# Performance work log

Hardware: AMD Instinct MI355X
Metric: run time of the kernel (lower is better)

Reference implementation:

```python
import jax, jax.numpy as jnp
import numpy as np

DIM = 256
EXP = 4
EPS_DYT = 1e-5
EPS_ATTN = 1e-5
TEMP = 10000.0


def _linear(x, w, b):
    # torch nn.Linear: y = x @ W^T + b, W is [out, in]
    return jnp.einsum('...i,oi->...o', x, w) + b


def _dwconv3x3(x_nhwc, w, b):
    # depthwise 3x3, padding=1; w: [C,1,3,3]
    xc = x_nhwc.transpose(0, 3, 1, 2)
    y = jax.lax.conv_general_dilated(
        xc, w, window_strides=(1, 1), padding='SAME',
        feature_group_count=w.shape[0],
        dimension_numbers=('NCHW', 'OIHW', 'NCHW'))
    return y.transpose(0, 2, 3, 1) + b


def _dyt(x, gamma, beta):
    mu = x.mean(axis=-1, keepdims=True)
    sd = x.std(axis=-1, keepdims=True, ddof=1) + EPS_DYT  # torch std is unbiased
    return jnp.tanh(gamma * (x - mu) / sd + beta)


def _mona(x, w, b):
    # SE-style: global avg pool -> fc -> sigmoid -> channel gate
    s = jax.nn.sigmoid(_linear(x.mean(axis=(1, 2)), w, b))  # [B,C]
    return x * s[:, None, None, :]


def _pos_emb(H, W, C):
    dq = C // 4
    omega = 1.0 / (TEMP ** (jnp.arange(dq, dtype=jnp.float32) / dq))
    xo = jnp.arange(W, dtype=jnp.float32)[:, None] * omega  # [W,dq]
    yo = jnp.arange(H, dtype=jnp.float32)[:, None] * omega  # [H,dq]
    xe = jnp.concatenate([jnp.sin(xo), jnp.cos(xo)], axis=-1)  # [W,2dq]
    ye = jnp.concatenate([jnp.sin(yo), jnp.cos(yo)], axis=-1)  # [H,2dq]
    pos = jnp.concatenate([
        jnp.broadcast_to(xe[None, :, :], (H, W, 2 * dq)),
        jnp.broadcast_to(ye[:, None, :], (H, W, 2 * dq))], axis=-1)  # [H,W,C]
    return pos


def setup_inputs() -> dict:
    key = jax.random.key(0)
    ks = jax.random.split(key, 16)
    d = DIM
    dh = d * EXP
    w = lambda k, shape: jax.random.normal(k, shape, dtype=jnp.float32) * 0.02
    return {
        'x': jax.random.normal(ks[0], (8, d // 4, 64, 64), dtype=jnp.float32),
        'in_proj_w': w(ks[1], (d, d // 4)),
        'wq_w': w(ks[2], (d, d)), 'wq_b': jnp.zeros((d,), jnp.float32),
        'wk_w': w(ks[3], (d, d)), 'wk_b': jnp.zeros((d,), jnp.float32),
        'wv_w': w(ks[4], (d, d)), 'wv_b': jnp.zeros((d,), jnp.float32),
        'wo_w': w(ks[5], (d, d)), 'wo_b': jnp.zeros((d,), jnp.float32),
        'psi_w': w(ks[6], (d, 1, 3, 3)), 'psi_b': jnp.zeros((d,), jnp.float32),
        'dyt_g': jnp.ones((d,), jnp.float32), 'dyt_b': jnp.zeros((d,), jnp.float32),
        'm1_w': w(ks[7], (d, d)), 'm1_b': jnp.zeros((d,), jnp.float32),
        'm2_w': w(ks[8], (d, d)), 'm2_b': jnp.zeros((d,), jnp.float32),
        'we_w': w(ks[9], (dh, d)), 'we_b': jnp.zeros((dh,), jnp.float32),
        'dw_w': w(ks[10], (dh, 1, 3, 3)), 'dw_b': jnp.zeros((dh,), jnp.float32),
        'wp_w': w(ks[11], (d, dh)), 'wp_b': jnp.zeros((d,), jnp.float32),
        'out_proj_w': w(ks[12], (d // 4, d)),
    }


def _sapa(x, wq_w, wq_b, wk_w, wk_b, wv_w, wv_b, wo_w, wo_b, psi_w, psi_b):
    B, H, W, C = x.shape
    N = H * W
    pos = _pos_emb(H, W, C).reshape(N, C)
    psi = jax.nn.sigmoid(_dwconv3x3(x, psi_w, psi_b)).reshape(B, N, C)
    xf = x.reshape(B, N, C)
    Q = psi * (_linear(xf, wq_w, wq_b) + pos)
    K = psi * (_linear(xf, wk_w, wk_b) + pos)
    V = _linear(xf, wv_w, wv_b)
    phi_Q = jnp.square(jax.nn.relu(Q))
    phi_K = jnp.square(jax.nn.relu(K))
    # attn / (phiQ @ sum_n phiK + eps) @ V  ==  (phiQ @ (phiK^T V)) / (phiQ @ ksum + eps)
    kv = jnp.einsum('bnc,bnd->bcd', phi_K, V)           # [B,C,C]
    num = jnp.einsum('bnc,bcd->bnd', phi_Q, kv)         # [B,N,C]
    den = jnp.einsum('bnc,bc->bn', phi_Q, phi_K.sum(axis=1))[..., None] + EPS_ATTN
    out = _linear(num / den, wo_w, wo_b)
    return out.reshape(B, H, W, C)


def _edffn(x, we_w, we_b, dw_w, dw_b, wp_w, wp_b):
    h = _linear(x, we_w, we_b)                 # [B,H,W,4C]
    h = jax.nn.gelu(_dwconv3x3(h, dw_w, dw_b))
    return x + _linear(h, wp_w, wp_b)


def reference(x, in_proj_w, wq_w, wq_b, wk_w, wk_b, wv_w, wv_b, wo_w, wo_b,
              psi_w, psi_b, dyt_g, dyt_b, m1_w, m1_b, m2_w, m2_b,
              we_w, we_b, dw_w, dw_b, wp_w, wp_b, out_proj_w):
    # in_proj: 1x1 conv (no bias; eval-BN is identity) + SiLU -> NHWC
    h = jax.nn.silu(jnp.einsum('bchw,oc->bhwo', x, in_proj_w))
    a = _sapa(h, wq_w, wq_b, wk_w, wk_b, wv_w, wv_b, wo_w, wo_b, psi_w, psi_b)
    U1 = _mona(_dyt(h + a, dyt_g, dyt_b), m1_w, m1_b)
    U2 = U1 + _edffn(U1, we_w, we_b, dw_w, dw_b, wp_w, wp_b)
    Y = _mona(_dyt(U2, dyt_g, dyt_b), m2_w, m2_b)
    return jax.nn.silu(jnp.einsum('bhwc,oc->bohw', Y, out_proj_w))
```

## Files before the change

kernel.cpp:

```cpp
#include <hip/hip_runtime.h>
#include <hip/hip_bf16.h>
#include <cmath>

using bf16 = __hip_bfloat16;
using bf16x8 = __attribute__((ext_vector_type(8))) short;
using bf16x4 = __attribute__((ext_vector_type(4))) short;
using f32x4v = __attribute__((ext_vector_type(4))) float;

static constexpr int BB  = 8;
static constexpr int HW  = 64;
static constexpr int NN  = HW * HW;
static constexpr int CC  = 256;
static constexpr int CIN = 64;
static constexpr int DH  = 1024;
static constexpr int MM  = BB * NN;

__device__ __forceinline__ bf16 f2b(float v) { return __float2bfloat16(v); }
__device__ __forceinline__ float b2f(bf16 v) { return __bfloat162float(v); }
__device__ __forceinline__ float tf(float v) { return v; }
__device__ __forceinline__ float tf(bf16 v)  { return b2f(v); }
__device__ __forceinline__ float frcp(float x) { return __builtin_amdgcn_rcpf(x); }
__device__ __forceinline__ float sigmf(float x) { return frcp(1.f + __expf(-x)); }
__device__ __forceinline__ float siluf(float x) { return x * sigmf(x); }
__device__ __forceinline__ float geluf(float x) {
  float z = x * fmaf(x * x, 0.07135481627f, 1.5957691216f);
  return x * sigmf(z);
}
__device__ __forceinline__ float tanhfast(float x) {
  return 1.f - 2.f * frcp(1.f + __expf(2.f * x));
}

__device__ __forceinline__ void stage16(const bf16* g, bf16* l) {
  __builtin_amdgcn_global_load_lds(
      (const __attribute__((address_space(1))) void*)g,
      (__attribute__((address_space(3))) void*)l, 16, 0, 0);
}

__global__ __launch_bounds__(256) void pos_kern(float* __restrict__ pos) {
  int n = blockIdx.x, o = threadIdx.x;
  int yy = n >> 6, xx = n & 63;
  int i = o & 63, q = o >> 6;
  float omega = __expf((float)i * -0.14391156831212787f);
  float coord = (q < 2) ? (float)xx : (float)yy;
  float ang = coord * omega;
  pos[(size_t)n * CC + o] = (q & 1) ? __cosf(ang) : __sinf(ang);
}

__global__ __launch_bounds__(256) void cvt_weights(
    const float* __restrict__ wq, const float* __restrict__ wk,
    const float* __restrict__ wv, const float* __restrict__ wo,
    const float* __restrict__ we, const float* __restrict__ wp,
    const float* __restrict__ qb, const float* __restrict__ kb,
    const float* __restrict__ vb,
    bf16* __restrict__ wqkvb, bf16* __restrict__ wob,
    bf16* __restrict__ web, bf16* __restrict__ wpb,
    float* __restrict__ bqkv, float* __restrict__ ksum) {
  int i = blockIdx.x * 256 + threadIdx.x;
  switch (blockIdx.y) {
    case 0: if (i < 65536) wqkvb[i] = f2b(wq[i]);
            if (i < 2048) ksum[i] = 0.f;
            break;
    case 1: if (i < 65536) wqkvb[65536 + i] = f2b(wk[i]);
            if (i < 768) bqkv[i] = (i < 256) ? qb[i] : (i < 512) ? kb[i - 256] : vb[i - 512];
            break;
    case 2: if (i < 65536) wqkvb[131072 + i] = f2b(wv[i]); break;
    case 3: if (i < 65536) wob[i] = f2b(wo[i]); break;
    case 4: web[i] = f2b(we[i]); break;
    case 5: wpb[i] = f2b(wp[i]); break;
  }
}

__global__ __launch_bounds__(256) void inproj_tile(const float* __restrict__ X,
                                                   const float* __restrict__ W,
                                                   float* __restrict__ H,
                                                   bf16* __restrict__ Hb) {
  __shared__ float Xs[16][68];
  __shared__ float Ws[16][68];
  int m0 = blockIdx.x * 64, o0 = blockIdx.y * 64, b = blockIdx.z;
  int tid = threadIdx.x, tx = tid & 15, ty = tid >> 4;
  float acc[4][4] = {};
  for (int k0 = 0; k0 < CIN; k0 += 16) {
    {
      int mm = tid & 63, kk0 = tid >> 6;
#pragma unroll
      for (int i = 0; i < 4; ++i) {
        int kk = kk0 * 4 + i;
        Xs[kk][mm] = X[((size_t)(b * CIN + k0 + kk)) * NN + m0 + mm];
      }
    }
    {
      int kk = tid & 15, oo0 = tid >> 4;
#pragma unroll
      for (int i = 0; i < 4; ++i) {
        int oo = oo0 + i * 16;
        Ws[kk][oo] = W[(size_t)(o0 + oo) * CIN + k0 + kk];
      }
    }
    __syncthreads();
#pragma unroll
    for (int kk = 0; kk < 16; ++kk) {
      float xv[4], wv[4];
#pragma unroll
      for (int a = 0; a < 4; ++a) xv[a] = Xs[kk][ty * 4 + a];
#pragma unroll
      for (int c = 0; c < 4; ++c) wv[c] = Ws[kk][tx * 4 + c];
#pragma unroll
      for (int a = 0; a < 4; ++a)
#pragma unroll
        for (int c = 0; c < 4; ++c) acc[a][c] += xv[a] * wv[c];
    }
    __syncthreads();
  }
#pragma unroll
  for (int a = 0; a < 4; ++a) {
    int m = m0 + ty * 4 + a;
#pragma unroll
    for (int c = 0; c < 4; ++c) {
      int o = o0 + tx * 4 + c;
      float v = siluf(acc[a][c]);
      size_t idx = ((size_t)b * NN + m) * CC + o;
      H[idx] = v;
      Hb[idx] = f2b(v);
    }
  }
}

__global__ __launch_bounds__(256) void outproj_tile(const float* __restrict__ T2,
                                                    const float* __restrict__ gate,
                                                    const float* __restrict__ W,
                                                    float* __restrict__ Y) {
  __shared__ float Xs[16][68];
  __shared__ float Ws[16][68];
  int n0 = blockIdx.x * 64, b = blockIdx.z;
  size_t mbase = (size_t)b * NN;
  const float* gb = gate + b * CC;
  int tid = threadIdx.x, tx = tid & 15, ty = tid >> 4;
  float acc[4][4] = {};
  for (int k0 = 0; k0 < CC; k0 += 16) {
    int kk = tid & 15, rr0 = tid >> 4;
    float gk = gb[k0 + kk];
#pragma unroll
    for (int i = 0; i < 4; ++i) {
      int rr = rr0 + i * 16;
      Xs[kk][rr] = T2[(mbase + n0 + rr) * CC + k0 + kk] * gk;
      Ws[kk][rr] = (rr < CIN) ? W[(size_t)rr * CC + k0 + kk] : 0.f;
    }
    __syncthreads();
#pragma unroll
    for (int kk2 = 0; kk2 < 16; ++kk2) {
      float xv[4], wv[4];
#pragma unroll
      for (int a = 0; a < 4; ++a) xv[a] = Xs[kk2][ty * 4 + a];
#pragma unroll
      for (int c = 0; c < 4; ++c) wv[c] = Ws[kk2][tx * 4 + c];
#pragma unroll
      for (int a = 0; a < 4; ++a)
#pragma unroll
        for (int c = 0; c < 4; ++c) acc[a][c] += xv[a] * wv[c];
    }
    __syncthreads();
  }
#pragma unroll
  for (int a = 0; a < 4; ++a) {
    int n = n0 + ty * 4 + a;
#pragma unroll
    for (int c = 0; c < 4; ++c) {
      int o = tx * 4 + c;
      if (o < CIN)
        Y[(size_t)(b * CIN + o) * NN + n] = siluf(acc[a][c]);
    }
  }
}

enum { EPI_PLAIN = 0, EPI_BIAS = 1, EPI_NUM = 3, EPI_RESID = 4, EPI_ADD1 = 5 };

__device__ __forceinline__ void storeO(float* p, float v) { *p = v; }
__device__ __forceinline__ void storeO(bf16* p, float v) { *p = f2b(v); }

template <int EPI, bool WPB, bool KVS, bool XSWZ, typename YT, typename A2T>
__global__ __launch_bounds__(256) void gemm_bf16(const bf16* __restrict__ X,
                                                 const bf16* __restrict__ W,
                                                 const float* __restrict__ bias,
                                                 YT* __restrict__ Y, int Kd, int Od,
                                                 const float* __restrict__ aux1,
                                                 const A2T* __restrict__ aux2) {
  __shared__ __align__(16) bf16 As[128 * 32];
  __shared__ __align__(16) bf16 Bs[128 * 32];
  int m0, o0;
  if (XSWZ) {
    int gy = gridDim.y;
    int nwg = gridDim.x * gy;
    int lin = blockIdx.y * gridDim.x + blockIdx.x;
    int q = nwg >> 3;
    int lin2 = (lin & 7) * q + (lin >> 3);
    m0 = (lin2 / gy) * 128;
    o0 = (lin2 % gy) * 128;
  } else {
    m0 = blockIdx.x * 128;
    o0 = blockIdx.y * 128;
  }
  int kbeg = 0, kend = Kd;
  if (KVS) {
    int b = blockIdx.z >> 4, ks = blockIdx.z & 15;
    size_t off = (size_t)b * CC * Kd;
    X += off; W += off;
    Y += (size_t)blockIdx.z * CC * CC;
    kbeg = ks * (Kd / 16); kend = kbeg + Kd / 16;
  }
  const bf16* Wp = WPB ? (W + (size_t)(m0 >> 12) * Kd * Od) : W;
  int t = threadIdx.x;
  int l = t & 63, w = t >> 6;
  int wm = (w >> 1) * 64, wn = (w & 1) * 64;
  int lr = l & 15, lq = l >> 4;
  int srow = t >> 2, skc = (t & 3) * 8;
  f32x4v acc[4][4] = {};
  for (int k0 = kbeg; k0 < kend; k0 += 32) {
    stage16(X + (size_t)(m0 + srow) * Kd + k0 + skc, As + t * 8);
    stage16(X + (size_t)(m0 + 64 + srow) * Kd + k0 + skc, As + 2048 + t * 8);
    stage16(Wp + (size_t)(o0 + srow) * Kd + k0 + skc, Bs + t * 8);
    stage16(Wp + (size_t)(o0 + 64 + srow) * Kd + k0 + skc, Bs + 2048 + t * 8);
    __syncthreads();
    bf16x8 af[4], bfr[4];
#pragma unroll
    for (int mt = 0; mt < 4; ++mt)
      af[mt] = *(const bf16x8*)(As + (wm + mt * 16 + lr) * 32 + lq * 8);
#pragma unroll
    for (int nt = 0; nt < 4; ++nt)
      bfr[nt] = *(const bf16x8*)(Bs + (wn + nt * 16 + lr) * 32 + lq * 8);
#pragma unroll
    for (int mt = 0; mt < 4; ++mt)
#pragma unroll
      for (int nt = 0; nt < 4; ++nt)
        acc[mt][nt] = __builtin_amdgcn_mfma_f32_16x16x32_bf16(af[mt], bfr[nt], acc[mt][nt], 0, 0, 0);
    __syncthreads();
  }
#pragma unroll
  for (int nt = 0; nt < 4; ++nt) {
    int o = o0 + wn + nt * 16 + lr;
    float bv = (EPI == EPI_PLAIN || EPI == EPI_NUM) ? 0.f : bias[o];
#pragma unroll
    for (int mt = 0; mt < 4; ++mt) {
      int mb = m0 + wm + mt * 16 + lq * 4;
#pragma unroll
      for (int r = 0; r < 4; ++r) {
        int m = mb + r;
        float v = acc[mt][nt][r] + bv;
        if constexpr (EPI == EPI_PLAIN || EPI == EPI_BIAS) {
          storeO(Y + (size_t)m * Od + o, v);
        } else if constexpr (EPI == EPI_NUM) {
          storeO(Y + (size_t)m * Od + o, v * aux1[m]);
        } else if constexpr (EPI == EPI_ADD1) {
          storeO(Y + (size_t)m * Od + o, v + tf(aux2[(size_t)m * Od + o]));
        } else {
          int gb = m >> 12;
          float u1 = tf(aux2[(size_t)m * Od + o]) * aux1[gb * CC + o];
          storeO(Y + (size_t)m * Od + o, v + 2.f * u1);
        }
      }
    }
  }
}

__global__ __launch_bounds__(256) void qkmath_kern(const bf16* __restrict__ QKV,
                                                   const float* __restrict__ pose,
                                                   const bf16* __restrict__ psi,
                                                   bf16* __restrict__ PQ,
                                                   bf16* __restrict__ KT,
                                                   bf16* __restrict__ VTo,
                                                   float* __restrict__ ksum) {
  __shared__ bf16 Ts[64][258];
  int sec = blockIdx.y;
  int m0 = blockIdx.x * 64;
  int b = m0 >> 12, n0 = m0 & (NN - 1);
  int t = threadIdx.x;
  int cg = (t & 31) * 8;
  int rg = t >> 5;
  if (sec == 0) {
#pragma unroll
    for (int p = 0; p < 8; ++p) {
      int r = p * 8 + rg;
      size_t m = (size_t)m0 + r;
      int n = (int)(m & (NN - 1));
      union { bf16x8 v; bf16 e[8]; } qv, pv, ov;
      qv.v = *(const bf16x8*)(QKV + m * 768 + cg);
      pv.v = *(const bf16x8*)(psi + m * CC + cg);
      const float* pr = pose + (size_t)n * CC + cg;
      f32x4v p0 = *(const f32x4v*)pr;
      f32x4v p1 = *(const f32x4v*)(pr + 4);
#pragma unroll
      for (int j = 0; j < 8; ++j) {
        float pj = (j < 4) ? p0[j] : p1[j - 4];
        float v = (b2f(qv.e[j]) + pj) * b2f(pv.e[j]);
        v = fmaxf(v, 0.f);
        ov.e[j] = f2b(v * v);
      }
      *(bf16x8*)(PQ + m * CC + cg) = ov.v;
    }
    return;
  }
  const bool KM = (sec == 1);
#pragma unroll
  for (int p = 0; p < 8; ++p) {
    int r = p * 8 + rg;
    size_t m = (size_t)m0 + r;
    union { bf16x8 v; bf16 e[8]; } qv, ov;
    qv.v = *(const bf16x8*)(QKV + m * 768 + sec * 256 + cg);
    if (KM) {
      int n = (int)(m & (NN - 1));
      union { bf16x8 v; bf16 e[8]; } pv;
      pv.v = *(const bf16x8*)(psi + m * CC + cg);
      const float* pr = pose + (size_t)n * CC + cg;
      f32x4v p0 = *(const f32x4v*)pr;
      f32x4v p1 = *(const f32x4v*)(pr + 4);
#pragma unroll
      for (int j = 0; j < 8; ++j) {
        float pj = (j < 4) ? p0[j] : p1[j - 4];
        float v = (b2f(qv.e[j]) + pj) * b2f(pv.e[j]);
        v = fmaxf(v, 0.f);
        ov.e[j] = f2b(v * v);
      }
    } else {
      ov.v = qv.v;
    }
    *(bf16x8*)(&Ts[r][cg]) = ov.v;
  }
  __syncthreads();
  int wv = t >> 6, lane = t & 63;
  bf16* base = KM ? KT : VTo;
  int nloc = (lane & 7) * 8;
  int gsub = lane >> 3;
#pragma unroll
  for (int k = 0; k < 8; ++k) {
    int c = wv * 64 + k * 8 + gsub;
    union { bf16x8 v; bf16 e[8]; } pk;
#pragma unroll
    for (int i = 0; i < 8; ++i) pk.e[i] = Ts[nloc + i][c];
    *(bf16x8*)(base + ((size_t)(b * CC + c)) * NN + n0 + nloc) = pk.v;
    if (KM) {
      float s = 0.f;
#pragma unroll
      for (int i = 0; i < 8; ++i) s += b2f(pk.e[i]);
      s += __shfl_xor(s, 1);
      s += __shfl_xor(s, 2);
      s += __shfl_xor(s, 4);
      if ((lane & 7) == 0) atomicAdd(&ksum[b * CC + c], s);
    }
  }
}

__global__ __launch_bounds__(256) void kvred_kern(const float* __restrict__ part,
                                                  bf16* __restrict__ kvTb) {
  int d = blockIdx.x, b = blockIdx.y, c = threadIdx.x;
  float s = 0.f;
#pragma unroll
  for (int ks = 0; ks < 16; ++ks)
    s += part[((size_t)(b * 16 + ks) * CC + d) * CC + c];
  kvTb[((size_t)b * CC + d) * CC + c] = f2b(s);
}

__global__ __launch_bounds__(256) void den_kern(const bf16* __restrict__ PQ,
                                                const float* __restrict__ ksum,
                                                float* __restrict__ rden) {
  int b = blockIdx.y;
  int n = blockIdx.x * 4 + (threadIdx.x >> 6);
  int lane = threadIdx.x & 63;
  size_t m = (size_t)b * NN + n;
  union { bf16x4 v; bf16 e[4]; } u;
  u.v = *(const bf16x4*)(PQ + m * CC + lane * 4);
  const float* ks = ksum + b * CC + lane * 4;
  float s = 0.f;
#pragma unroll
  for (int j = 0; j < 4; ++j) s += b2f(u.e[j]) * ks[j];
#pragma unroll
  for (int off = 32; off >= 1; off >>= 1) s += __shfl_down(s, off);
  if (lane == 0) rden[m] = 1.f / (s + 1e-5f);
}

template <bool RESID>
__global__ __launch_bounds__(256) void dyt_kern(const float* __restrict__ X,
                                                const float* __restrict__ R,
                                                const float* __restrict__ g,
                                                const float* __restrict__ bt,
                                                float* __restrict__ T,
                                                float* __restrict__ poolq) {
  int wv = threadIdx.x >> 6;
  int m = blockIdx.x * 4 + wv;
  int lane = threadIdx.x & 63;
  size_t base = (size_t)m * CC + lane * 4;
  f32x4v x = *(const f32x4v*)(X + base);
  if constexpr (RESID) {
    f32x4v r = *(const f32x4v*)(R + base);
#pragma unroll
    for (int j = 0; j < 4; ++j) x[j] += r[j];
  }
  float s = (x[0] + x[1]) + (x[2] + x[3]);
  float q = fmaf(x[0], x[0], fmaf(x[1], x[1], fmaf(x[2], x[2], x[3] * x[3])));
#pragma unroll
  for (int off = 32; off >= 1; off >>= 1) {
    s += __shfl_xor(s, off);
    q += __shfl_xor(q, off);
  }
  float mu = s * (1.f / 256.f);
  float var = (q - 256.f * mu * mu) * (1.f / 255.f);
  float sd = sqrtf(fmaxf(var, 0.f)) + 1e-5f;
  float rs = frcp(sd);
  f32x4v gv = *(const f32x4v*)(g + lane * 4);
  f32x4v bv = *(const f32x4v*)(bt + lane * 4);
  f32x4v o;
#pragma unroll
  for (int j = 0; j < 4; ++j)
    o[j] = tanhfast(fmaf(gv[j] * (x[j] - mu), rs, bv[j]));
  *(f32x4v*)(T + base) = o;
  __shared__ float ps[4][260];
#pragma unroll
  for (int j = 0; j < 4; ++j) ps[wv][lane * 4 + j] = o[j];
  __syncthreads();
  if (wv == 0) {
    f32x4v pv;
#pragma unroll
    for (int j = 0; j < 4; ++j) {
      int c = lane * 4 + j;
      pv[j] = (ps[0][c] + ps[1][c]) + (ps[2][c] + ps[3][c]);
    }
    *(f32x4v*)(poolq + (size_t)blockIdx.x * 256 + lane * 4) = pv;
  }
}

__global__ __launch_bounds__(256) void poolred_kern(const float* __restrict__ poolq,
                                                    float* __restrict__ pool16) {
  int s = blockIdx.x, b = blockIdx.y, c = threadIdx.x;
  float acc = 0.f;
#pragma unroll 8
  for (int k = 0; k < 64; ++k)
    acc += poolq[((size_t)(b * 1024 + s * 64 + k)) * 256 + c];
  pool16[(size_t)(b * 16 + s) * 256 + c] = acc;
}

__global__ __launch_bounds__(256) void gate_kern(const float* __restrict__ pool16,
                                                 const float* __restrict__ w,
                                                 const float* __restrict__ bias,
                                                 float* __restrict__ gate) {
  int b = blockIdx.x, o = threadIdx.x;
  __shared__ float p[CC];
  float s = 0.f;
#pragma unroll
  for (int k = 0; k < 16; ++k) s += pool16[(size_t)(b * 16 + k) * 256 + o];
  p[o] = s * (1.f / 4096.f);
  __syncthreads();
  float acc = bias[o];
  for (int c = 0; c < CC; ++c) acc += p[c] * w[o * CC + c];
  gate[b * CC + o] = sigmf(acc);
}

__global__ __launch_bounds__(256) void scale_b16(const float* __restrict__ T,
                                                 const float* __restrict__ gate,
                                                 bf16* __restrict__ Ob) {
  size_t i4 = ((size_t)blockIdx.x * 256 + threadIdx.x) * 4;
  int b = (int)(i4 >> 20);
  int c = (int)(i4 & (CC - 1));
  f32x4v t = *(const f32x4v*)(T + i4);
  f32x4v gv = *(const f32x4v*)(gate + b * CC + c);
  union { bf16x4 v; bf16 e[4]; } ob;
#pragma unroll
  for (int j = 0; j < 4; ++j) ob.e[j] = f2b(t[j] * gv[j]);
  *(bf16x4*)(Ob + i4) = ob.v;
}

__device__ __forceinline__ void dw_loadrow_bf16(float (&row)[3][4], const bf16* __restrict__ Xb,
                                                int yy, int x, int dl, int dr) {
  if (yy < 0 || yy >= HW) {
#pragma unroll
    for (int cx = 0; cx < 3; ++cx)
#pragma unroll
      for (int j = 0; j < 4; ++j) row[cx][j] = 0.f;
    return;
  }
  const bf16* base = Xb + ((size_t)yy * HW + x) * (size_t)DH;
  union U { bf16x4 v; bf16 e[4]; } um, ul, ur;
  um.v = *(const bf16x4*)base;
  ul.v = *(const bf16x4*)(base + dl);
  ur.v = *(const bf16x4*)(base + dr);
#pragma unroll
  for (int j = 0; j < 4; ++j) {
    row[0][j] = b2f(ul.e[j]);
    row[1][j] = b2f(um.e[j]);
    row[2][j] = b2f(ur.e[j]);
  }
}

__device__ __forceinline__ void dw_loadrow_f32(float (&row)[3][4], const float* __restrict__ Xb,
                                               int yy, int x, int dl, int dr) {
  if (yy < 0 || yy >= HW) {
#pragma unroll
    for (int cx = 0; cx < 3; ++cx)
#pragma unroll
      for (int j = 0; j < 4; ++j) row[cx][j] = 0.f;
    return;
  }
  const float* base = Xb + ((size_t)yy * HW + x) * (size_t)CC;
  f32x4v m = *(const f32x4v*)base;
  f32x4v lf = *(const f32x4v*)(base + dl);
  f32x4v rg = *(const f32x4v*)(base + dr);
#pragma unroll
  for (int j = 0; j < 4; ++j) {
    row[0][j] = lf[j];
    row[1][j] = m[j];
    row[2][j] = rg[j];
  }
}

__global__ __launch_bounds__(256) void dwconv_psi_v2(const float* __restrict__ X,
                                                     const float* __restrict__ w,
                                                     const float* __restrict__ bias,
                                                     bf16* __restrict__ Y) {
  int i = blockIdx.x;
  int lin = (i & 7) * 64 + (i >> 3);
  int xg = lin & 15, yc = (lin >> 4) & 3, b = lin >> 6;
  int c0 = (threadIdx.x & 63) * 4;
  int x  = xg * 4 + (threadIdx.x >> 6);
  int y0 = yc * 16;
  const float* Xb = X + (size_t)b * NN * CC + c0;
  bf16* Yb       = Y + (size_t)b * NN * CC + c0;
  float wt[9][4], bs[4];
#pragma unroll
  for (int j = 0; j < 4; ++j) {
    bs[j] = bias[c0 + j];
#pragma unroll
    for (int t9 = 0; t9 < 9; ++t9) wt[t9][j] = w[(c0 + j) * 9 + t9];
  }
  const bool xl = (x > 0), xr = (x < HW - 1);
  if (!xl) {
#pragma unroll
    for (int j = 0; j < 4; ++j) wt[0][j] = wt[3][j] = wt[6][j] = 0.f;
  }
  if (!xr) {
#pragma unroll
    for (int j = 0; j < 4; ++j) wt[2][j] = wt[5][j] = wt[8][j] = 0.f;
  }
  const int dl = xl ? -CC : 0, dr = xr ? CC : 0;
  float win[5][3][4];
  dw_loadrow_f32(win[0], Xb, y0 - 1, x, dl, dr);
  dw_loadrow_f32(win[1], Xb, y0,     x, dl, dr);
  dw_loadrow_f32(win[2], Xb, y0 + 1, x, dl, dr);
  dw_loadrow_f32(win[3], Xb, y0 + 2, x, dl, dr);
#pragma unroll
  for (int ii = 0; ii < 16; ++ii) {
    dw_loadrow_f32(win[(ii + 4) % 5], Xb, y0 + ii + 3, x, dl, dr);
    const int rt = ii % 5, rm = (ii + 1) % 5, rb = (ii + 2) % 5;
    union { bf16x4 v; bf16 e[4]; } o;
#pragma unroll
    for (int j = 0; j < 4; ++j) {
      float a = bs[j];
#pragma unroll
      for (int cx = 0; cx < 3; ++cx) {
        a = fmaf(win[rt][cx][j], wt[cx][j], a);
        a = fmaf(win[rm][cx][j], wt[3 + cx][j], a);
        a = fmaf(win[rb][cx][j], wt[6 + cx][j], a);
      }
      o.e[j] = f2b(sigmf(a));
    }
    *(bf16x4*)(Yb + ((size_t)(y0 + ii) * HW + x) * (size_t)CC) = o.v;
  }
}

__global__ __launch_bounds__(256) void dwconv1024_v2(const bf16* __restrict__ X,
                                                     const float* __restrict__ w,
                                                     const float* __restrict__ bias,
                                                     bf16* __restrict__ Y) {
  int i = blockIdx.x;
  int lin = (i & 7) * 256 + (i >> 3);
  int x = lin & 63, yc = (lin >> 6) & 3, b = lin >> 8;
  int c0 = threadIdx.x * 4;
  int y0 = yc * 16;
  const bf16* Xb = X + (size_t)b * NN * DH + c0;
  bf16* Yb       = Y + (size_t)b * NN * DH + c0;
  float wt[9][4], bs[4];
#pragma unroll
  for (int j = 0; j < 4; ++j) {
    bs[j] = bias[c0 + j];
#pragma unroll
    for (int t9 = 0; t9 < 9; ++t9) wt[t9][j] = w[(c0 + j) * 9 + t9];
  }
  const bool xl = (x > 0), xr = (x < HW - 1);
  if (!xl) {
#pragma unroll
    for (int j = 0; j < 4; ++j) wt[0][j] = wt[3][j] = wt[6][j] = 0.f;
  }
  if (!xr) {
#pragma unroll
    for (int j = 0; j < 4; ++j) wt[2][j] = wt[5][j] = wt[8][j] = 0.f;
  }
  const int dl = xl ? -DH : 0, dr = xr ? DH : 0;
  float win[5][3][4];
  dw_loadrow_bf16(win[0], Xb, y0 - 1, x, dl, dr);
  dw_loadrow_bf16(win[1], Xb, y0,     x, dl, dr);
  dw_loadrow_bf16(win[2], Xb, y0 + 1, x, dl, dr);
  dw_loadrow_bf16(win[3], Xb, y0 + 2, x, dl, dr);
#pragma unroll
  for (int ii = 0; ii < 16; ++ii) {
    dw_loadrow_bf16(win[(ii + 4) % 5], Xb, y0 + ii + 3, x, dl, dr);
    const int rt = ii % 5, rm = (ii + 1) % 5, rb = (ii + 2) % 5;
    union { bf16x4 v; bf16 e[4]; } o;
#pragma unroll
    for (int j = 0; j < 4; ++j) {
      float a = bs[j];
#pragma unroll
      for (int cx = 0; cx < 3; ++cx) {
        a = fmaf(win[rt][cx][j], wt[cx][j], a);
        a = fmaf(win[rm][cx][j], wt[3 + cx][j], a);
        a = fmaf(win[rb][cx][j], wt[6 + cx][j], a);
      }
      o.e[j] = f2b(geluf(a));
    }
    *(bf16x4*)(Yb + ((size_t)(y0 + ii) * HW + x) * (size_t)DH) = o.v;
  }
}

extern "C" void kernel_launch(void* const* d_in, const int* in_sizes, int n_in,
                              void* d_out, int out_size, void* d_ws, size_t ws_size,
                              hipStream_t stream) {
  (void)in_sizes; (void)n_in; (void)out_size; (void)ws_size;
  const float* x       = (const float*)d_in[0];
  const float* in_proj = (const float*)d_in[1];
  const float* wq_w = (const float*)d_in[2];   const float* wq_b = (const float*)d_in[3];
  const float* wk_w = (const float*)d_in[4];   const float* wk_b = (const float*)d_in[5];
  const float* wv_w = (const float*)d_in[6];   const float* wv_b = (const float*)d_in[7];
  const float* wo_w = (const float*)d_in[8];   const float* wo_b = (const float*)d_in[9];
  const float* psi_w = (const float*)d_in[10]; const float* psi_b = (const float*)d_in[11];
  const float* dyt_g = (const float*)d_in[12]; const float* dyt_b = (const float*)d_in[13];
  const float* m1_w = (const float*)d_in[14];  const float* m1_b = (const float*)d_in[15];
  const float* m2_w = (const float*)d_in[16];  const float* m2_b = (const float*)d_in[17];
  const float* we_w = (const float*)d_in[18];  const float* we_b = (const float*)d_in[19];
  const float* dw_w = (const float*)d_in[20];  const float* dw_b = (const float*)d_in[21];
  const float* wp_w = (const float*)d_in[22];  const float* wp_b = (const float*)d_in[23];
  const float* wout = (const float*)d_in[24];
  float* out = (float*)d_out;

  char* ws = (char*)d_ws;
  const size_t MB = 1u << 20;
  float* H     = (float*)(ws);
  float* T1    = (float*)(ws);
  float* A     = (float*)(ws + 32 * MB);
  bf16*  psiB  = (bf16*)(ws + 64 * MB);
  bf16*  numb  = (bf16*)(ws + 80 * MB);
  bf16*  phiQ  = (bf16*)(ws + 96 * MB);
  bf16*  Hb    = (bf16*)(ws + 112 * MB);
  bf16*  phiKT = (bf16*)(ws + 128 * MB);
  bf16*  VT    = (bf16*)(ws + 144 * MB);
  bf16*  QKVr  = (bf16*)(ws + 160 * MB);
  float* kvpart = (float*)(ws + 160 * MB);
  bf16*  e1    = (bf16*)(ws + 64 * MB);
  bf16*  e2    = (bf16*)(ws + 128 * MB);
  float* T2    = (float*)(ws + 64 * MB);
  bf16*  U1b   = (bf16*)(ws + 192 * MB);
  bf16* wqkvb = (bf16*)(ws + 208 * MB);
  bf16* wob   = wqkvb + 196608;
  bf16* web   = wob + 65536;
  bf16* wpb   = web + 262144;
  float* bqkv = (float*)(wpb + 262144);
  float* pose = (float*)(ws + 210 * MB);
  char*  small = ws + 214 * MB;
  float* ksum  = (float*)(small);
  float* rden  = (float*)(small + 64 * 1024);
  float* pool16 = (float*)(small + 192 * 1024);
  float* gate1 = (float*)(small + 704 * 1024);
  float* gate2 = (float*)(small + 720 * 1024);
  bf16*  kvTb  = (bf16*)(small + 768 * 1024);
  float* poolq = (float*)(ws + 216 * MB);

  dim3 blk(256);

  pos_kern<<<dim3(NN), blk, 0, stream>>>(pose);
  cvt_weights<<<dim3(1024, 6), blk, 0, stream>>>(wq_w, wk_w, wv_w, wo_w, we_w, wp_w,
                                                 wq_b, wk_b, wv_b,
                                                 wqkvb, wob, web, wpb, bqkv, ksum);
  inproj_tile<<<dim3(64, 4, BB), blk, 0, stream>>>(x, in_proj, H, Hb);

  dwconv_psi_v2<<<dim3(512), blk, 0, stream>>>(H, psi_w, psi_b, psiB);
  gemm_bf16<EPI_BIAS, false, false, true, bf16, float>
      <<<dim3(256, 6), blk, 0, stream>>>(Hb, wqkvb, bqkv, QKVr, CC, 768, nullptr, nullptr);
  qkmath_kern<<<dim3(MM / 64, 3), blk, 0, stream>>>(QKVr, pose, psiB, phiQ, phiKT, VT, ksum);
  gemm_bf16<EPI_PLAIN, false, true, false, float, float>
      <<<dim3(2, 2, 128), blk, 0, stream>>>(VT, phiKT, nullptr, kvpart, NN, CC, nullptr, nullptr);
  kvred_kern<<<dim3(CC, BB), blk, 0, stream>>>(kvpart, kvTb);
  den_kern<<<dim3(1024, BB), blk, 0, stream>>>(phiQ, ksum, rden);
  gemm_bf16<EPI_NUM, true, false, true, bf16, float>
      <<<dim3(256, 2), blk, 0, stream>>>(phiQ, kvTb, nullptr, numb, CC, CC, rden, nullptr);
  gemm_bf16<EPI_ADD1, false, false, true, float, float>
      <<<dim3(256, 2), blk, 0, stream>>>(numb, wob, wo_b, A, CC, CC, nullptr, H);

  dyt_kern<false><<<dim3(MM / 4), blk, 0, stream>>>(A, nullptr, dyt_g, dyt_b, T1, poolq);
  poolred_kern<<<dim3(16, BB), blk, 0, stream>>>(poolq, pool16);
  gate_kern<<<dim3(BB), blk, 0, stream>>>(pool16, m1_w, m1_b, gate1);
  scale_b16<<<dim3(MM / 4), blk, 0, stream>>>(T1, gate1, U1b);

  gemm_bf16<EPI_BIAS, false, false, true, bf16, float>
      <<<dim3(256, 8), blk, 0, stream>>>(U1b, web, we_b, e1, CC, DH, nullptr, nullptr);
  dwconv1024_v2<<<dim3(2048), blk, 0, stream>>>(e1, dw_w, dw_b, e2);
  gemm_bf16<EPI_RESID, false, false, true, float, float>
      <<<dim3(256, 2), blk, 0, stream>>>(e2, wpb, wp_b, A, DH, CC, gate1, T1);

  dyt_kern<false><<<dim3(MM / 4), blk, 0, stream>>>(A, nullptr, dyt_g, dyt_b, T2, poolq);
  poolred_kern<<<dim3(16, BB), blk, 0, stream>>>(poolq, pool16);
  gate_kern<<<dim3(BB), blk, 0, stream>>>(pool16, m2_w, m2_b, gate2);

  outproj_tile<<<dim3(64, 1, BB), blk, 0, stream>>>(T2, gate2, wout, out);
}
```

Measured before the change: 444.7 us.

## Use 64-row GEMM tiles for narrow outputs, bf16 inputs for psi conv and kv partials

Adds a BM64 variant of the bf16 MFMA GEMM that uses 64-row tiles with four warps split along N. It is applied to the three GEMMs with 256-wide outputs, doubling their grid to 1024 blocks and improving occupancy across CUs. The psi depthwise conv now reads the bf16 copy of H instead of fp32, and the kv split-K partials are stored as bf16, halving traffic on those paths. The cost is less reuse of W tiles per block and extra rounding in the kv partial sums.

```diff
diff --git a/kernel.cpp b/kernel.cpp
--- a/kernel.cpp
+++ b/kernel.cpp
@@ -177,14 +177,16 @@
 __device__ __forceinline__ void storeO(float* p, float v) { *p = v; }
 __device__ __forceinline__ void storeO(bf16* p, float v) { *p = f2b(v); }
 
-template <int EPI, bool WPB, bool KVS, bool XSWZ, typename YT, typename A2T>
+template <int EPI, bool WPB, bool KVS, bool XSWZ, bool BM64, typename YT, typename A2T>
 __global__ __launch_bounds__(256) void gemm_bf16(const bf16* __restrict__ X,
                                                  const bf16* __restrict__ W,
                                                  const float* __restrict__ bias,
                                                  YT* __restrict__ Y, int Kd, int Od,
                                                  const float* __restrict__ aux1,
                                                  const A2T* __restrict__ aux2) {
-  __shared__ __align__(16) bf16 As[128 * 32];
+  constexpr int BM  = BM64 ? 64 : 128;
+  constexpr int NNT = BM64 ? 2 : 4;
+  __shared__ __align__(16) bf16 As[BM * 32];
   __shared__ __align__(16) bf16 Bs[128 * 32];
   int m0, o0;
   if (XSWZ) {
@@ -193,10 +195,10 @@
     int lin = blockIdx.y * gridDim.x + blockIdx.x;
     int q = nwg >> 3;
     int lin2 = (lin & 7) * q + (lin >> 3);
-    m0 = (lin2 / gy) * 128;
+    m0 = (lin2 / gy) * BM;
     o0 = (lin2 % gy) * 128;
   } else {
-    m0 = blockIdx.x * 128;
+    m0 = blockIdx.x * BM;
     o0 = blockIdx.y * 128;
   }
   int kbeg = 0, kend = Kd;
@@ -210,32 +212,34 @@
   const bf16* Wp = WPB ? (W + (size_t)(m0 >> 12) * Kd * Od) : W;
   int t = threadIdx.x;
   int l = t & 63, w = t >> 6;
-  int wm = (w >> 1) * 64, wn = (w & 1) * 64;
+  int wm = BM64 ? 0 : (w >> 1) * 64;
+  int wn = BM64 ? w * 32 : (w & 1) * 64;
   int lr = l & 15, lq = l >> 4;
   int srow = t >> 2, skc = (t & 3) * 8;
-  f32x4v acc[4][4] = {};
+  f32x4v acc[4][NNT] = {};
   for (int k0 = kbeg; k0 < kend; k0 += 32) {
     stage16(X + (size_t)(m0 + srow) * Kd + k0 + skc, As + t * 8);
-    stage16(X + (size_t)(m0 + 64 + srow) * Kd + k0 + skc, As + 2048 + t * 8);
+    if (!BM64)
+      stage16(X + (size_t)(m0 + 64 + srow) * Kd + k0 + skc, As + 2048 + t * 8);
     stage16(Wp + (size_t)(o0 + srow) * Kd + k0 + skc, Bs + t * 8);
     stage16(Wp + (size_t)(o0 + 64 + srow) * Kd + k0 + skc, Bs + 2048 + t * 8);
     __syncthreads();
-    bf16x8 af[4], bfr[4];
+    bf16x8 af[4], bfr[NNT];
 #pragma unroll
     for (int mt = 0; mt < 4; ++mt)
       af[mt] = *(const bf16x8*)(As + (wm + mt * 16 + lr) * 32 + lq * 8);
 #pragma unroll
-    for (int nt = 0; nt < 4; ++nt)
+    for (int nt = 0; nt < NNT; ++nt)
       bfr[nt] = *(const bf16x8*)(Bs + (wn + nt * 16 + lr) * 32 + lq * 8);
 #pragma unroll
     for (int mt = 0; mt < 4; ++mt)
 #pragma unroll
-      for (int nt = 0; nt < 4; ++nt)
+      for (int nt = 0; nt < NNT; ++nt)
         acc[mt][nt] = __builtin_amdgcn_mfma_f32_16x16x32_bf16(af[mt], bfr[nt], acc[mt][nt], 0, 0, 0);
     __syncthreads();
   }
 #pragma unroll
-  for (int nt = 0; nt < 4; ++nt) {
+  for (int nt = 0; nt < NNT; ++nt) {
     int o = o0 + wn + nt * 16 + lr;
     float bv = (EPI == EPI_PLAIN || EPI == EPI_NUM) ? 0.f : bias[o];
 #pragma unroll
@@ -348,13 +352,13 @@
   }
 }
 
-__global__ __launch_bounds__(256) void kvred_kern(const float* __restrict__ part,
+__global__ __launch_bounds__(256) void kvred_kern(const bf16* __restrict__ part,
                                                   bf16* __restrict__ kvTb) {
   int d = blockIdx.x, b = blockIdx.y, c = threadIdx.x;
   float s = 0.f;
 #pragma unroll
   for (int ks = 0; ks < 16; ++ks)
-    s += part[((size_t)(b * 16 + ks) * CC + d) * CC + c];
+    s += b2f(part[((size_t)(b * 16 + ks) * CC + d) * CC + c]);
   kvTb[((size_t)b * CC + d) * CC + c] = f2b(s);
 }
 
@@ -466,8 +470,9 @@
   *(bf16x4*)(Ob + i4) = ob.v;
 }
 
-__device__ __forceinline__ void dw_loadrow_bf16(float (&row)[3][4], const bf16* __restrict__ Xb,
-                                                int yy, int x, int dl, int dr) {
+template <int STRIDE>
+__device__ __forceinline__ void dw_loadrow_b16(float (&row)[3][4], const bf16* __restrict__ Xb,
+                                               int yy, int x, int dl, int dr) {
   if (yy < 0 || yy >= HW) {
 #pragma unroll
     for (int cx = 0; cx < 3; ++cx)
@@ -475,7 +480,7 @@
       for (int j = 0; j < 4; ++j) row[cx][j] = 0.f;
     return;
   }
-  const bf16* base = Xb + ((size_t)yy * HW + x) * (size_t)DH;
+  const bf16* base = Xb + ((size_t)yy * HW + x) * (size_t)STRIDE;
   union U { bf16x4 v; bf16 e[4]; } um, ul, ur;
   um.v = *(const bf16x4*)base;
   ul.v = *(const bf16x4*)(base + dl);
@@ -488,28 +493,7 @@
   }
 }
 
-__device__ __forceinline__ void dw_loadrow_f32(float (&row)[3][4], const float* __restrict__ Xb,
-                                               int yy, int x, int dl, int dr) {
-  if (yy < 0 || yy >= HW) {
-#pragma unroll
-    for (int cx = 0; cx < 3; ++cx)
-#pragma unroll
-      for (int j = 0; j < 4; ++j) row[cx][j] = 0.f;
-    return;
-  }
-  const float* base = Xb + ((size_t)yy * HW + x) * (size_t)CC;
-  f32x4v m = *(const f32x4v*)base;
-  f32x4v lf = *(const f32x4v*)(base + dl);
-  f32x4v rg = *(const f32x4v*)(base + dr);
-#pragma unroll
-  for (int j = 0; j < 4; ++j) {
-    row[0][j] = lf[j];
-    row[1][j] = m[j];
-    row[2][j] = rg[j];
-  }
-}
-
-__global__ __launch_bounds__(256) void dwconv_psi_v2(const float* __restrict__ X,
+__global__ __launch_bounds__(256) void dwconv_psi_v2(const bf16* __restrict__ X,
                                                      const float* __restrict__ w,
                                                      const float* __restrict__ bias,
                                                      bf16* __restrict__ Y) {
@@ -519,8 +503,8 @@
   int c0 = (threadIdx.x & 63) * 4;
   int x  = xg * 4 + (threadIdx.x >> 6);
   int y0 = yc * 16;
-  const float* Xb = X + (size_t)b * NN * CC + c0;
-  bf16* Yb       = Y + (size_t)b * NN * CC + c0;
+  const bf16* Xb = X + (size_t)b * NN * CC + c0;
+  bf16* Yb      = Y + (size_t)b * NN * CC + c0;
   float wt[9][4], bs[4];
 #pragma unroll
   for (int j = 0; j < 4; ++j) {
@@ -539,13 +523,13 @@
   }
   const int dl = xl ? -CC : 0, dr = xr ? CC : 0;
   float win[5][3][4];
-  dw_loadrow_f32(win[0], Xb, y0 - 1, x, dl, dr);
-  dw_loadrow_f32(win[1], Xb, y0,     x, dl, dr);
-  dw_loadrow_f32(win[2], Xb, y0 + 1, x, dl, dr);
-  dw_loadrow_f32(win[3], Xb, y0 + 2, x, dl, dr);
+  dw_loadrow_b16<CC>(win[0], Xb, y0 - 1, x, dl, dr);
+  dw_loadrow_b16<CC>(win[1], Xb, y0,     x, dl, dr);
+  dw_loadrow_b16<CC>(win[2], Xb, y0 + 1, x, dl, dr);
+  dw_loadrow_b16<CC>(win[3], Xb, y0 + 2, x, dl, dr);
 #pragma unroll
   for (int ii = 0; ii < 16; ++ii) {
-    dw_loadrow_f32(win[(ii + 4) % 5], Xb, y0 + ii + 3, x, dl, dr);
+    dw_loadrow_b16<CC>(win[(ii + 4) % 5], Xb, y0 + ii + 3, x, dl, dr);
     const int rt = ii % 5, rm = (ii + 1) % 5, rb = (ii + 2) % 5;
     union { bf16x4 v; bf16 e[4]; } o;
 #pragma unroll
@@ -592,13 +576,13 @@
   }
   const int dl = xl ? -DH : 0, dr = xr ? DH : 0;
   float win[5][3][4];
-  dw_loadrow_bf16(win[0], Xb, y0 - 1, x, dl, dr);
-  dw_loadrow_bf16(win[1], Xb, y0,     x, dl, dr);
-  dw_loadrow_bf16(win[2], Xb, y0 + 1, x, dl, dr);
-  dw_loadrow_bf16(win[3], Xb, y0 + 2, x, dl, dr);
+  dw_loadrow_b16<DH>(win[0], Xb, y0 - 1, x, dl, dr);
+  dw_loadrow_b16<DH>(win[1], Xb, y0,     x, dl, dr);
+  dw_loadrow_b16<DH>(win[2], Xb, y0 + 1, x, dl, dr);
+  dw_loadrow_b16<DH>(win[3], Xb, y0 + 2, x, dl, dr);
 #pragma unroll
   for (int ii = 0; ii < 16; ++ii) {
-    dw_loadrow_bf16(win[(ii + 4) % 5], Xb, y0 + ii + 3, x, dl, dr);
+    dw_loadrow_b16<DH>(win[(ii + 4) % 5], Xb, y0 + ii + 3, x, dl, dr);
     const int rt = ii % 5, rm = (ii + 1) % 5, rb = (ii + 2) % 5;
     union { bf16x4 v; bf16 e[4]; } o;
 #pragma unroll
@@ -648,7 +632,7 @@
   bf16*  phiKT = (bf16*)(ws + 128 * MB);
   bf16*  VT    = (bf16*)(ws + 144 * MB);
   bf16*  QKVr  = (bf16*)(ws + 160 * MB);
-  float* kvpart = (float*)(ws + 160 * MB);
+  bf16*  kvpartB = (bf16*)(ws + 160 * MB);
   bf16*  e1    = (bf16*)(ws + 64 * MB);
   bf16*  e2    = (bf16*)(ws + 128 * MB);
   float* T2    = (float*)(ws + 64 * MB);
@@ -676,29 +660,29 @@
                                                  wqkvb, wob, web, wpb, bqkv, ksum);
   inproj_tile<<<dim3(64, 4, BB), blk, 0, stream>>>(x, in_proj, H, Hb);
 
-  dwconv_psi_v2<<<dim3(512), blk, 0, stream>>>(H, psi_w, psi_b, psiB);
-  gemm_bf16<EPI_BIAS, false, false, true, bf16, float>
+  dwconv_psi_v2<<<dim3(512), blk, 0, stream>>>(Hb, psi_w, psi_b, psiB);
+  gemm_bf16<EPI_BIAS, false, false, true, false, bf16, float>
       <<<dim3(256, 6), blk, 0, stream>>>(Hb, wqkvb, bqkv, QKVr, CC, 768, nullptr, nullptr);
   qkmath_kern<<<dim3(MM / 64, 3), blk, 0, stream>>>(QKVr, pose, psiB, phiQ, phiKT, VT, ksum);
-  gemm_bf16<EPI_PLAIN, false, true, false, float, float>
-      <<<dim3(2, 2, 128), blk, 0, stream>>>(VT, phiKT, nullptr, kvpart, NN, CC, nullptr, nullptr);
-  kvred_kern<<<dim3(CC, BB), blk, 0, stream>>>(kvpart, kvTb);
+  gemm_bf16<EPI_PLAIN, false, true, false, false, bf16, float>
+      <<<dim3(2, 2, 128), blk, 0, stream>>>(VT, phiKT, nullptr, kvpartB, NN, CC, nullptr, nullptr);
+  kvred_kern<<<dim3(CC, BB), blk, 0, stream>>>(kvpartB, kvTb);
   den_kern<<<dim3(1024, BB), blk, 0, stream>>>(phiQ, ksum, rden);
-  gemm_bf16<EPI_NUM, true, false, true, bf16, float>
-      <<<dim3(256, 2), blk, 0, stream>>>(phiQ, kvTb, nullptr, numb, CC, CC, rden, nullptr);
-  gemm_bf16<EPI_ADD1, false, false, true, float, float>
-      <<<dim3(256, 2), blk, 0, stream>>>(numb, wob, wo_b, A, CC, CC, nullptr, H);
+  gemm_bf16<EPI_NUM, true, false, true, true, bf16, float>
+      <<<dim3(512, 2), blk, 0, stream>>>(phiQ, kvTb, nullptr, numb, CC, CC, rden, nullptr);
+  gemm_bf16<EPI_ADD1, false, false, true, true, float, float>
+      <<<dim3(512, 2), blk, 0, stream>>>(numb, wob, wo_b, A, CC, CC, nullptr, H);
 
   dyt_kern<false><<<dim3(MM / 4), blk, 0, stream>>>(A, nullptr, dyt_g, dyt_b, T1, poolq);
   poolred_kern<<<dim3(16, BB), blk, 0, stream>>>(poolq, pool16);
   gate_kern<<<dim3(BB), blk, 0, stream>>>(pool16, m1_w, m1_b, gate1);
   scale_b16<<<dim3(MM / 4), blk, 0, stream>>>(T1, gate1, U1b);
 
-  gemm_bf16<EPI_BIAS, false, false, true, bf16, float>
+  gemm_bf16<EPI_BIAS, false, false, true, false, bf16, float>
       <<<dim3(256, 8), blk, 0, stream>>>(U1b, web, we_b, e1, CC, DH, nullptr, nullptr);
   dwconv1024_v2<<<dim3(2048), blk, 0, stream>>>(e1, dw_w, dw_b, e2);
-  gemm_bf16<EPI_RESID, false, false, true, float, float>
-      <<<dim3(256, 2), blk, 0, stream>>>(e2, wpb, wp_b, A, DH, CC, gate1, T1);
+  gemm_bf16<EPI_RESID, false, false, true, true, float, float>
+      <<<dim3(512, 2), blk, 0, stream>>>(e2, wpb, wp_b, A, DH, CC, gate1, T1);
 
   dyt_kern<false><<<dim3(MM / 4), blk, 0, stream>>>(A, nullptr, dyt_g, dyt_b, T2, poolq);
   poolred_kern<<<dim3(16, BB), blk, 0, stream>>>(poolq, pool16);
```

After: 448.7 us. About the same (+0.9%).
